# Optimization experiments

Hardware: AMD Instinct MI355X
Metric: run time of the kernel (lower is better)

The kernel has to match this reference:

```python
import jax, jax.numpy as jnp
import numpy as np

BLOCK = 64   # init block_size
RATIO = 0.5  # init ratio
GRAY = 128.0


def _make_mask(depth_map, H, W, key):
    """Vectorized equivalent of the per-block python loop.

    Blocks with initial_mask > ratio are kept (all ones). Dropped blocks are
    filled with a random binary region containing round(depth*b*b) zeros,
    chosen uniformly without replacement (torch.randperm semantics ==
    rank-of-uniform-noise < num_zeros).
    """
    nH, nW = H // BLOCK, W // BLOCK
    k1, k2 = jax.random.split(key)
    initial_mask = jax.random.uniform(k1, (nH, nW))           # [nH,nW]
    keep = initial_mask > RATIO                                # blocks kept fully

    d = jnp.where(depth_map.max() > 1.0, depth_map / 255.0, depth_map)
    gray_depth = d.mean(axis=0)                                # [H,W]
    # avg_pool2d with kernel=stride=BLOCK
    avg_depth = gray_depth.reshape(nH, BLOCK, nW, BLOCK).mean(axis=(1, 3))  # [nH,nW]
    num_zeros = jnp.round(avg_depth * (BLOCK * BLOCK)).astype(jnp.int32)    # per block

    # random permutation rank per pixel within each block
    noise = jax.random.uniform(k2, (nH, nW, BLOCK * BLOCK))
    ranks = jnp.argsort(jnp.argsort(noise, axis=-1), axis=-1)               # [nH,nW,b*b]
    region = (ranks >= num_zeros[..., None]).astype(jnp.float32)            # zeros at low ranks

    blocks = jnp.where(keep[..., None], 1.0, region)           # [nH,nW,b*b]
    mask = blocks.reshape(nH, nW, BLOCK, BLOCK).transpose(0, 2, 1, 3).reshape(H, W)
    return mask


def setup_inputs() -> dict:
    key = jax.random.key(0)
    k1, k2 = jax.random.split(key)
    img = jax.random.uniform(k1, (3, 2048, 4096), dtype=jnp.float32) * 255.0
    depth_map = jax.random.uniform(k2, (3, 2048, 4096), dtype=jnp.float32)
    return {"img": img, "depth_map": depth_map}


def reference(img, depth_map):
    C, H, W = img.shape
    mask = _make_mask(depth_map, H, W, jax.random.key(42))     # [H,W]
    # resize to (H,W) is a no-op since mask is already full resolution
    return img * mask + GRAY * (1.0 - mask)
```

## Files before the change

kernel.cpp:

```cpp
#include <hip/hip_runtime.h>
#include <stdint.h>

static constexpr int kH  = 2048;
static constexpr int kW  = 4096;
static constexpr int kHW = kH * kW;
static constexpr int kNH = kH / 64;
static constexpr int kNW = kW / 64;
static constexpr int kNB = kNH * kNW;
static constexpr int kBB = 64 * 64;
static constexpr int kGrayN = kNB * kBB;
static constexpr float kGray = 128.0f;

__host__ __device__ inline void tf2x32(uint32_t k0, uint32_t k1,
                                       uint32_t x0, uint32_t x1,
                                       uint32_t& o0, uint32_t& o1) {
  uint32_t ks2 = 0x1BD11BDAu ^ k0 ^ k1;
  x0 += k0; x1 += k1;
#define ROTL(v, d) (((v) << (d)) | ((v) >> (32 - (d))))
#define RND(R) { x0 += x1; x1 = ROTL(x1, R); x1 ^= x0; }
  RND(13) RND(15) RND(26) RND(6)
  x0 += k1;  x1 += ks2 + 1u;
  RND(17) RND(29) RND(16) RND(24)
  x0 += ks2; x1 += k0 + 2u;
  RND(13) RND(15) RND(26) RND(6)
  x0 += k0;  x1 += k1 + 3u;
  RND(17) RND(29) RND(16) RND(24)
  x0 += k1;  x1 += ks2 + 4u;
  RND(13) RND(15) RND(26) RND(6)
  x0 += ks2; x1 += k0 + 5u;
  o0 = x0; o1 = x1;
#undef RND
#undef ROTL
}

__device__ inline uint32_t rbits(uint32_t ka, uint32_t kb, uint32_t idx) {
  uint32_t o0, o1;
  tf2x32(ka, kb, 0u, idx, o0, o1);
  return o0 ^ o1;
}

__device__ inline bool keep_block(uint32_t k1a, uint32_t k1b, int b) {
  uint32_t v = rbits(k1a, k1b, (uint32_t)b) >> 9;
  return v > 0x400000u;
}

__global__ __launch_bounds__(256) void k1_depth(const float* __restrict__ depth,
                                                float* __restrict__ Gu,
                                                float* __restrict__ Gs,
                                                float* __restrict__ Bmax,
                                                uint32_t k1a, uint32_t k1b_) {
  __shared__ float red[256];
  const int b = blockIdx.x, t = threadIdx.x;
  const int bi = b >> 6, bj = b & 63;
  const int y0 = bi * 64, x0 = bj * 64;
  const bool keep = keep_block(k1a, k1b_, b);
  const float4* d4 = reinterpret_cast<const float4*>(depth);

  float mx = 0.0f;
  #pragma unroll
  for (int it = 0; it < 4; ++it) {
    int idx = it * 256 + t;
    int r = idx >> 4, cq = idx & 15;
    uint32_t a4 = (uint32_t)(y0 + r) * (kW / 4) + (uint32_t)(x0 / 4 + cq);
    float4 d0 = d4[a4];
    float4 d1 = d4[a4 + kHW / 4];
    float4 d2 = d4[a4 + 2 * (kHW / 4)];
    mx = fmaxf(mx, fmaxf(fmaxf(fmaxf(d0.x, d0.y), fmaxf(d0.z, d0.w)),
               fmaxf(fmaxf(fmaxf(d1.x, d1.y), fmaxf(d1.z, d1.w)),
                     fmaxf(fmaxf(d2.x, d2.y), fmaxf(d2.z, d2.w)))));
    if (!keep) {
      uint32_t p4 = (uint32_t)b * (kBB / 4) + (uint32_t)idx;
      float4 u, s;
      u.x = ((d0.x + d1.x) + d2.x) / 3.0f;
      u.y = ((d0.y + d1.y) + d2.y) / 3.0f;
      u.z = ((d0.z + d1.z) + d2.z) / 3.0f;
      u.w = ((d0.w + d1.w) + d2.w) / 3.0f;
      s.x = ((d0.x / 255.0f + d1.x / 255.0f) + d2.x / 255.0f) / 3.0f;
      s.y = ((d0.y / 255.0f + d1.y / 255.0f) + d2.y / 255.0f) / 3.0f;
      s.z = ((d0.z / 255.0f + d1.z / 255.0f) + d2.z / 255.0f) / 3.0f;
      s.w = ((d0.w / 255.0f + d1.w / 255.0f) + d2.w / 255.0f) / 3.0f;
      reinterpret_cast<float4*>(Gu)[p4] = u;
      reinterpret_cast<float4*>(Gs)[p4] = s;
    }
  }
  red[t] = mx;
  __syncthreads();
  for (int s = 128; s > 0; s >>= 1) {
    if (t < s) red[t] = fmaxf(red[t], red[t + s]);
    __syncthreads();
  }
  if (t == 0) Bmax[b] = red[0];
}

__global__ __launch_bounds__(64) void kchain(const float* __restrict__ G,
                                             const float* __restrict__ Bmax,
                                             float* __restrict__ S,
                                             uint32_t k1a, uint32_t k1b_) {
  const int w = blockIdx.x, lane = threadIdx.x;

  float m = 0.0f;
  #pragma unroll
  for (int i = 0; i < kNB / 64; ++i) m = fmaxf(m, Bmax[lane + i * 64]);
  #pragma unroll
  for (int d = 32; d >= 1; d >>= 1) m = fmaxf(m, __shfl_xor(m, d, 64));
  const bool flag = m > 1.0f;

  uint32_t bits = 0; int c = 0;
  #pragma unroll
  for (int j = 0; j < 32; ++j) {
    int b = lane * 32 + j;
    if (!keep_block(k1a, k1b_, b)) { bits |= (1u << j); ++c; }
  }
  int P = c;
  #pragma unroll
  for (int d = 1; d < 64; d <<= 1) {
    int v = __shfl_up(P, d, 64);
    if (lane >= d) P += v;
  }
  const int total = __shfl(P, 63, 64);
  P -= c;
  const int r0 = 2 * w, r1 = 2 * w + 1;
  int b0c = -1, b1c = -1;
  if (r0 >= P && r0 < P + c) {
    uint32_t bb = bits;
    for (int i = r0 - P; i > 0; --i) bb &= bb - 1;
    b0c = lane * 32 + __ffs(bb) - 1;
  }
  if (r1 >= P && r1 < P + c) {
    uint32_t bb = bits;
    for (int i = r1 - P; i > 0; --i) bb &= bb - 1;
    b1c = lane * 32 + __ffs(bb) - 1;
  }
  unsigned long long m0 = __ballot(b0c >= 0);
  unsigned long long m1 = __ballot(b1c >= 0);
  const int blk0 = (r0 < total && m0) ? __shfl(b0c, (int)(__ffsll(m0) - 1), 64) : -1;
  const int blk1 = (r1 < total && m1) ? __shfl(b1c, (int)(__ffsll(m1) - 1), 64) : -1;

  const int blk = (lane == 0) ? blk0 : blk1;
  if (lane < 2 && blk >= 0) {
    const float4* g4 = reinterpret_cast<const float4*>(G) +
                       (flag ? (uint32_t)(kGrayN / 4) : 0u) + (uint32_t)blk * (kBB / 4);
    float4 buf[32];
    #pragma unroll
    for (int i = 0; i < 32; ++i) buf[i] = g4[i];
    uint32_t gp = 32;
    float acc = 0.0f;
    for (int outer = 0; outer < 31; ++outer) {
      #pragma unroll
      for (int i = 0; i < 32; ++i) {
        float4 v = buf[i];
        buf[i] = g4[gp + i];
        acc += v.x; acc += v.y; acc += v.z; acc += v.w;
      }
      gp += 32;
    }
    #pragma unroll
    for (int i = 0; i < 32; ++i) {
      float4 v = buf[i];
      acc += v.x; acc += v.y; acc += v.z; acc += v.w;
    }
    S[blk] = acc;
  }
}

__global__ __launch_bounds__(256) void k3_fused(const float* __restrict__ img,
                                                float* __restrict__ out,
                                                const float* __restrict__ S,
                                                uint32_t k1a, uint32_t k1b_,
                                                uint32_t k2a, uint32_t k2b) {
  __shared__ uint32_t hist[256];
  __shared__ uint32_t cand[64];
  __shared__ uint32_t sh[4];
  __shared__ uint32_t wtot[4];
  const int b = blockIdx.x, t = threadIdx.x;
  const int lane = t & 63, wv = t >> 6;
  const int bi = b >> 6, bj = b & 63;
  const int y0 = bi * 64, x0 = bj * 64;
  const float4* img4 = reinterpret_cast<const float4*>(img);
  float4* out4 = reinterpret_cast<float4*>(out);

  int nz;
  if (keep_block(k1a, k1b_, b)) {
    nz = 0;
  } else {
    float sv = S[b];
    nz = (int)rintf(sv);
    if (nz < 0) nz = 0;
    if (nz > kBB) nz = kBB;
  }
  const int row0 = t >> 4, cq = t & 15;

  if (nz == 0 || nz == kBB) {
    const bool fill = (nz == kBB);
    const float4 g4v = make_float4(kGray, kGray, kGray, kGray);
    #pragma unroll
    for (int i = 0; i < 12; ++i) {
      int f = i * 256 + t;
      int ch = f >> 10, idx = f & 1023;
      int r = idx >> 4, cc = idx & 15;
      uint32_t a = (uint32_t)(y0 + r) * (kW / 4) + (uint32_t)(x0 / 4 + cc)
                 + (uint32_t)ch * (kHW / 4);
      out4[a] = fill ? g4v : img4[a];
    }
    return;
  }

  const uint32_t base = (uint32_t)b * (uint32_t)kBB;
  uint32_t v[4][4];
  #pragma unroll
  for (int it = 0; it < 4; ++it) {
    uint32_t p = (uint32_t)((it * 16 + row0) * 64 + cq * 4);
    #pragma unroll
    for (int j = 0; j < 4; ++j) v[it][j] = rbits(k2a, k2b, base + p + j) >> 9;
  }

  hist[t] = 0;
  if (t == 0) sh[3] = 0;
  __syncthreads();
  #pragma unroll
  for (int it = 0; it < 4; ++it)
    #pragma unroll
    for (int j = 0; j < 4; ++j) atomicAdd(&hist[v[it][j] >> 15], 1u);
  __syncthreads();
  {
    uint32_t h = hist[t], sc = h;
    #pragma unroll
    for (int d = 1; d < 64; d <<= 1) {
      uint32_t vv = __shfl_up(sc, d, 64);
      if (lane >= d) sc += vv;
    }
    if (lane == 63) wtot[wv] = sc;
    __syncthreads();
    uint32_t pre = 0;
    for (int k = 0; k < wv; ++k) pre += wtot[k];
    uint32_t inc = sc + pre, exc = inc - h;
    if (inc >= (uint32_t)nz && exc < (uint32_t)nz) { sh[0] = (uint32_t)t; sh[1] = (uint32_t)nz - exc; }
    hist[t] = 0;
    __syncthreads();
  }
  const uint32_t B1 = sh[0], rr2 = sh[1];

  #pragma unroll
  for (int it = 0; it < 4; ++it)
    #pragma unroll
    for (int j = 0; j < 4; ++j) {
      uint32_t vv = v[it][j];
      if ((vv >> 15) == B1) atomicAdd(&hist[(vv >> 7) & 0xFFu], 1u);
    }
  __syncthreads();
  {
    uint32_t h = hist[t], sc = h;
    #pragma unroll
    for (int d = 1; d < 64; d <<= 1) {
      uint32_t vv = __shfl_up(sc, d, 64);
      if (lane >= d) sc += vv;
    }
    if (lane == 63) wtot[wv] = sc;
    __syncthreads();
    uint32_t pre = 0;
    for (int k = 0; k < wv; ++k) pre += wtot[k];
    uint32_t inc = sc + pre, exc = inc - h;
    if (inc >= rr2 && exc < rr2) { sh[0] = (uint32_t)t; sh[1] = rr2 - exc; }
    __syncthreads();
  }
  const uint32_t pref16 = (B1 << 8) | sh[0];
  const uint32_t rr3 = sh[1];

  #pragma unroll
  for (int it = 0; it < 4; ++it)
    #pragma unroll
    for (int j = 0; j < 4; ++j) {
      uint32_t vv = v[it][j];
      if ((vv >> 7) == pref16) {
        uint32_t p = (uint32_t)((it * 16 + row0) * 64 + cq * 4 + j);
        uint32_t slot = atomicAdd(&sh[3], 1u);
        if (slot < 64u) cand[slot] = ((vv & 0x7Fu) << 12) | p;
      }
    }
  __syncthreads();
  const uint32_t m = sh[3] < 64u ? sh[3] : 64u;
  if (t < (int)m) {
    uint32_t key = cand[t], rank = 0;
    for (uint32_t q = 0; q < m; ++q) rank += (cand[q] < key) ? 1u : 0u;
    if (rank == rr3 - 1) sh[2] = key;
  }
  __syncthreads();
  const uint32_t T3 = sh[2];

  #pragma unroll
  for (int it = 0; it < 4; ++it) {
    uint32_t p = (uint32_t)((it * 16 + row0) * 64 + cq * 4);
    uint32_t kmask = 0;
    #pragma unroll
    for (int j = 0; j < 4; ++j) {
      uint32_t vv = v[it][j];
      uint32_t pre = vv >> 7;
      bool zero = (pre < pref16) ||
                  (pre == pref16 && ((((vv & 0x7Fu) << 12) | (p + j)) <= T3));
      if (!zero) kmask |= (1u << j);
    }
    uint32_t a4 = (uint32_t)(y0 + it * 16 + row0) * (kW / 4) + (uint32_t)(x0 / 4 + cq);
    #pragma unroll
    for (int ch = 0; ch < 3; ++ch) {
      uint32_t a = a4 + (uint32_t)ch * (kHW / 4);
      float4 vf = img4[a];
      float4 o;
      o.x = (kmask & 1u) ? vf.x : kGray;
      o.y = (kmask & 2u) ? vf.y : kGray;
      o.z = (kmask & 4u) ? vf.z : kGray;
      o.w = (kmask & 8u) ? vf.w : kGray;
      out4[a] = o;
    }
  }
}

extern "C" void kernel_launch(void* const* d_in, const int* in_sizes, int n_in,
                              void* d_out, int out_size, void* d_ws, size_t ws_size,
                              hipStream_t stream) {
  const float* img   = (const float*)d_in[0];
  const float* depth = (const float*)d_in[1];
  float* out = (float*)d_out;

  float* Gu = out;
  float* Gs = out + kGrayN;

  float* S    = (float*)d_ws;
  float* Bmax = S + kNB;

  uint32_t k1a, k1b_, k2a, k2b;
  tf2x32(0u, 42u, 0u, 0u, k1a, k1b_);
  tf2x32(0u, 42u, 0u, 1u, k2a, k2b);

  k1_depth<<<kNB, 256, 0, stream>>>(depth, Gu, Gs, Bmax, k1a, k1b_);
  kchain  <<<kNB / 2, 64, 0, stream>>>(out, Bmax, S, k1a, k1b_);
  k3_fused<<<kNB, 256, 0, stream>>>(img, out, S, k1a, k1b_, k2a, k2b);
}
```

Measured before the change: 112.8 us.

## Fuse block-sum chain kernel into the final masking kernel

Removes the separate kchain kernel. Its per-block depth sum is now computed by one lane inside the final kernel, and it runs alongside the RNG and histogram work. The intermediate gray-depth values are written straight into the output buffer at the block's own spatial location, which drops the compaction indexing and the extra workspace array. Kept blocks exit early with a plain copy. The cost is a long serial single-lane reduction that holds up each dropped block's workgroup at the barrier, in exchange for one fewer kernel launch and no inter-kernel dependency.

```diff
diff --git a/kernel.cpp b/kernel.cpp
--- a/kernel.cpp
+++ b/kernel.cpp
@@ -8,7 +8,6 @@
 static constexpr int kNW = kW / 64;
 static constexpr int kNB = kNH * kNW;
 static constexpr int kBB = 64 * 64;
-static constexpr int kGrayN = kNB * kBB;
 static constexpr float kGray = 128.0f;
 
 __host__ __device__ inline void tf2x32(uint32_t k0, uint32_t k1,
@@ -45,8 +44,7 @@
 }
 
 __global__ __launch_bounds__(256) void k1_depth(const float* __restrict__ depth,
-                                                float* __restrict__ Gu,
-                                                float* __restrict__ Gs,
+                                                float* __restrict__ out,
                                                 float* __restrict__ Bmax,
                                                 uint32_t k1a, uint32_t k1b_) {
   __shared__ float red[256];
@@ -55,6 +53,7 @@
   const int y0 = bi * 64, x0 = bj * 64;
   const bool keep = keep_block(k1a, k1b_, b);
   const float4* d4 = reinterpret_cast<const float4*>(depth);
+  float4* out4 = reinterpret_cast<float4*>(out);
 
   float mx = 0.0f;
   #pragma unroll
@@ -69,7 +68,6 @@
                fmaxf(fmaxf(fmaxf(d1.x, d1.y), fmaxf(d1.z, d1.w)),
                      fmaxf(fmaxf(d2.x, d2.y), fmaxf(d2.z, d2.w)))));
     if (!keep) {
-      uint32_t p4 = (uint32_t)b * (kBB / 4) + (uint32_t)idx;
       float4 u, s;
       u.x = ((d0.x + d1.x) + d2.x) / 3.0f;
       u.y = ((d0.y + d1.y) + d2.y) / 3.0f;
@@ -79,8 +77,8 @@
       s.y = ((d0.y / 255.0f + d1.y / 255.0f) + d2.y / 255.0f) / 3.0f;
       s.z = ((d0.z / 255.0f + d1.z / 255.0f) + d2.z / 255.0f) / 3.0f;
       s.w = ((d0.w / 255.0f + d1.w / 255.0f) + d2.w / 255.0f) / 3.0f;
-      reinterpret_cast<float4*>(Gu)[p4] = u;
-      reinterpret_cast<float4*>(Gs)[p4] = s;
+      out4[a4] = u;
+      out4[a4 + kHW / 4] = s;
     }
   }
   red[t] = mx;
@@ -92,86 +90,16 @@
   if (t == 0) Bmax[b] = red[0];
 }
 
-__global__ __launch_bounds__(64) void kchain(const float* __restrict__ G,
-                                             const float* __restrict__ Bmax,
-                                             float* __restrict__ S,
-                                             uint32_t k1a, uint32_t k1b_) {
-  const int w = blockIdx.x, lane = threadIdx.x;
-
-  float m = 0.0f;
-  #pragma unroll
-  for (int i = 0; i < kNB / 64; ++i) m = fmaxf(m, Bmax[lane + i * 64]);
-  #pragma unroll
-  for (int d = 32; d >= 1; d >>= 1) m = fmaxf(m, __shfl_xor(m, d, 64));
-  const bool flag = m > 1.0f;
-
-  uint32_t bits = 0; int c = 0;
-  #pragma unroll
-  for (int j = 0; j < 32; ++j) {
-    int b = lane * 32 + j;
-    if (!keep_block(k1a, k1b_, b)) { bits |= (1u << j); ++c; }
-  }
-  int P = c;
-  #pragma unroll
-  for (int d = 1; d < 64; d <<= 1) {
-    int v = __shfl_up(P, d, 64);
-    if (lane >= d) P += v;
-  }
-  const int total = __shfl(P, 63, 64);
-  P -= c;
-  const int r0 = 2 * w, r1 = 2 * w + 1;
-  int b0c = -1, b1c = -1;
-  if (r0 >= P && r0 < P + c) {
-    uint32_t bb = bits;
-    for (int i = r0 - P; i > 0; --i) bb &= bb - 1;
-    b0c = lane * 32 + __ffs(bb) - 1;
-  }
-  if (r1 >= P && r1 < P + c) {
-    uint32_t bb = bits;
-    for (int i = r1 - P; i > 0; --i) bb &= bb - 1;
-    b1c = lane * 32 + __ffs(bb) - 1;
-  }
-  unsigned long long m0 = __ballot(b0c >= 0);
-  unsigned long long m1 = __ballot(b1c >= 0);
-  const int blk0 = (r0 < total && m0) ? __shfl(b0c, (int)(__ffsll(m0) - 1), 64) : -1;
-  const int blk1 = (r1 < total && m1) ? __shfl(b1c, (int)(__ffsll(m1) - 1), 64) : -1;
-
-  const int blk = (lane == 0) ? blk0 : blk1;
-  if (lane < 2 && blk >= 0) {
-    const float4* g4 = reinterpret_cast<const float4*>(G) +
-                       (flag ? (uint32_t)(kGrayN / 4) : 0u) + (uint32_t)blk * (kBB / 4);
-    float4 buf[32];
-    #pragma unroll
-    for (int i = 0; i < 32; ++i) buf[i] = g4[i];
-    uint32_t gp = 32;
-    float acc = 0.0f;
-    for (int outer = 0; outer < 31; ++outer) {
-      #pragma unroll
-      for (int i = 0; i < 32; ++i) {
-        float4 v = buf[i];
-        buf[i] = g4[gp + i];
-        acc += v.x; acc += v.y; acc += v.z; acc += v.w;
-      }
-      gp += 32;
-    }
-    #pragma unroll
-    for (int i = 0; i < 32; ++i) {
-      float4 v = buf[i];
-      acc += v.x; acc += v.y; acc += v.z; acc += v.w;
-    }
-    S[blk] = acc;
-  }
-}
-
-__global__ __launch_bounds__(256) void k3_fused(const float* __restrict__ img,
-                                                float* __restrict__ out,
-                                                const float* __restrict__ S,
-                                                uint32_t k1a, uint32_t k1b_,
-                                                uint32_t k2a, uint32_t k2b) {
+__global__ __launch_bounds__(256) void k3_mega(const float* __restrict__ img,
+                                               float* __restrict__ out,
+                                               const float* __restrict__ Bmax,
+                                               uint32_t k1a, uint32_t k1b_,
+                                               uint32_t k2a, uint32_t k2b) {
   __shared__ uint32_t hist[256];
   __shared__ uint32_t cand[64];
   __shared__ uint32_t sh[4];
   __shared__ uint32_t wtot[4];
+  __shared__ float sacc;
   const int b = blockIdx.x, t = threadIdx.x;
   const int lane = t & 63, wv = t >> 6;
   const int bi = b >> 6, bj = b & 63;
@@ -179,16 +107,72 @@
   const float4* img4 = reinterpret_cast<const float4*>(img);
   float4* out4 = reinterpret_cast<float4*>(out);
 
+  if (keep_block(k1a, k1b_, b)) {
+    #pragma unroll
+    for (int i = 0; i < 12; ++i) {
+      int f = i * 256 + t;
+      int ch = f >> 10, idx = f & 1023;
+      int r = idx >> 4, cc = idx & 15;
+      uint32_t a = (uint32_t)(y0 + r) * (kW / 4) + (uint32_t)(x0 / 4 + cc)
+                 + (uint32_t)ch * (kHW / 4);
+      out4[a] = img4[a];
+    }
+    return;
+  }
+
+  hist[t] = 0;
+  if (t == 0) sh[3] = 0;
+  __syncthreads();
+
+  if (wv == 0) {
+    float m = 0.0f;
+    #pragma unroll
+    for (int i = 0; i < kNB / 64; ++i) m = fmaxf(m, Bmax[lane + i * 64]);
+    #pragma unroll
+    for (int d = 32; d >= 1; d >>= 1) m = fmaxf(m, __shfl_xor(m, d, 64));
+    const bool flag = m > 1.0f;
+    if (lane == 0) {
+      const float4* base4 = out4 + (uint32_t)y0 * (kW / 4) + (uint32_t)(x0 / 4)
+                          + (flag ? (uint32_t)(kHW / 4) : 0u);
+      float acc = 0.0f;
+      for (int row = 0; row < 64; ++row) {
+        const float4* rp = base4 + (uint32_t)row * (kW / 4);
+        float4 a[8];
+        #pragma unroll
+        for (int i = 0; i < 8; ++i) a[i] = rp[i];
+        #pragma unroll
+        for (int i = 0; i < 8; ++i) { acc += a[i].x; acc += a[i].y; acc += a[i].z; acc += a[i].w; }
+        #pragma unroll
+        for (int i = 0; i < 8; ++i) a[i] = rp[8 + i];
+        #pragma unroll
+        for (int i = 0; i < 8; ++i) { acc += a[i].x; acc += a[i].y; acc += a[i].z; acc += a[i].w; }
+      }
+      sacc = acc;
+    }
+  }
+
+  const int row0 = t >> 4, cq = t & 15;
+  const uint32_t base = (uint32_t)b * (uint32_t)kBB;
+  uint32_t v[4][4];
+  #pragma unroll
+  for (int it = 0; it < 4; ++it) {
+    uint32_t p = (uint32_t)((it * 16 + row0) * 64 + cq * 4);
+    #pragma unroll
+    for (int j = 0; j < 4; ++j) v[it][j] = rbits(k2a, k2b, base + p + j) >> 9;
+  }
+  #pragma unroll
+  for (int it = 0; it < 4; ++it)
+    #pragma unroll
+    for (int j = 0; j < 4; ++j) atomicAdd(&hist[v[it][j] >> 15], 1u);
+  __syncthreads();
+
   int nz;
-  if (keep_block(k1a, k1b_, b)) {
-    nz = 0;
-  } else {
-    float sv = S[b];
+  {
+    float sv = sacc;
     nz = (int)rintf(sv);
     if (nz < 0) nz = 0;
     if (nz > kBB) nz = kBB;
   }
-  const int row0 = t >> 4, cq = t & 15;
 
   if (nz == 0 || nz == kBB) {
     const bool fill = (nz == kBB);
@@ -205,23 +189,6 @@
     return;
   }
 
-  const uint32_t base = (uint32_t)b * (uint32_t)kBB;
-  uint32_t v[4][4];
-  #pragma unroll
-  for (int it = 0; it < 4; ++it) {
-    uint32_t p = (uint32_t)((it * 16 + row0) * 64 + cq * 4);
-    #pragma unroll
-    for (int j = 0; j < 4; ++j) v[it][j] = rbits(k2a, k2b, base + p + j) >> 9;
-  }
-
-  hist[t] = 0;
-  if (t == 0) sh[3] = 0;
-  __syncthreads();
-  #pragma unroll
-  for (int it = 0; it < 4; ++it)
-    #pragma unroll
-    for (int j = 0; j < 4; ++j) atomicAdd(&hist[v[it][j] >> 15], 1u);
-  __syncthreads();
   {
     uint32_t h = hist[t], sc = h;
     #pragma unroll
@@ -321,17 +288,12 @@
   const float* depth = (const float*)d_in[1];
   float* out = (float*)d_out;
 
-  float* Gu = out;
-  float* Gs = out + kGrayN;
-
-  float* S    = (float*)d_ws;
-  float* Bmax = S + kNB;
+  float* Bmax = (float*)d_ws;
 
   uint32_t k1a, k1b_, k2a, k2b;
   tf2x32(0u, 42u, 0u, 0u, k1a, k1b_);
   tf2x32(0u, 42u, 0u, 1u, k2a, k2b);
 
-  k1_depth<<<kNB, 256, 0, stream>>>(depth, Gu, Gs, Bmax, k1a, k1b_);
-  kchain  <<<kNB / 2, 64, 0, stream>>>(out, Bmax, S, k1a, k1b_);
-  k3_fused<<<kNB, 256, 0, stream>>>(img, out, S, k1a, k1b_, k2a, k2b);
-}
+  k1_depth<<<kNB, 256, 0, stream>>>(depth, out, Bmax, k1a, k1b_);
+  k3_mega <<<kNB, 256, 0, stream>>>(img, out, Bmax, k1a, k1b_, k2a, k2b);
+}
```

Result: slower. 119.5 us (+6.0%).
